# Performance work log

Hardware: AMD Instinct MI355X
Metric: run time of the kernel (lower is better)

## Reference

```python
import jax, jax.numpy as jnp
import numpy as np

B, NQ, NK, D = 8, 2048, 2048, 512

def setup_inputs() -> dict:
    key = jax.random.key(0)
    ks = jax.random.split(key, 6)
    s = 1.0 / np.sqrt(D)
    return {
        "query": jax.random.normal(ks[0], (B, NQ, D), dtype=jnp.float32),
        "key":   jax.random.normal(ks[1], (B, NK, D), dtype=jnp.float32),
        "value": jax.random.normal(ks[2], (B, NK, D), dtype=jnp.float32),
        "Wq": jax.random.normal(ks[3], (D, D), dtype=jnp.float32) * s,
        "Wk": jax.random.normal(ks[4], (D, D), dtype=jnp.float32) * s,
        "Wv": jax.random.normal(ks[5], (D, D), dtype=jnp.float32) * s,
    }

def reference(query, key, value, Wq, Wk, Wv):
    # nn.Linear(bias=False): y = x @ W.T
    q = jnp.einsum('bnd,ed->bne', query, Wq)
    k = jnp.einsum('bnd,ed->bne', key, Wk)
    v = jnp.einsum('bnd,ed->bne', value, Wv)
    # NOTE: original module applies NO 1/sqrt(d) scaling
    scores = jnp.einsum('bqd,bkd->bqk', q, k)   # [B, NQ, NK]
    weights = jax.nn.softmax(scores, axis=-1)
    return jnp.einsum('bqk,bkd->bqd', weights, v)
```

## Files before the change

kernel.cpp:

```cpp
#include <hip/hip_runtime.h>

typedef __attribute__((ext_vector_type(8))) short short8;
typedef __attribute__((ext_vector_type(8))) _Float16 half8;
typedef __attribute__((ext_vector_type(4))) float f32x4;
typedef __attribute__((ext_vector_type(4))) unsigned short u16x4;
typedef __attribute__((ext_vector_type(4))) _Float16 half4;

#define NB 8
#define NQL 2048
#define NKL 2048
#define DD 512

static __device__ __forceinline__ void stage16(const void* g, void* l){
  __builtin_amdgcn_global_load_lds(
      (const __attribute__((address_space(1))) void*)g,
      (__attribute__((address_space(3))) void*)l, 16, 0, 0);
}

static __device__ __forceinline__ void barrier_lgkm(){
  asm volatile("s_waitcnt lgkmcnt(0)" ::: "memory");
  __builtin_amdgcn_s_barrier();
  asm volatile("" ::: "memory");
}

static __device__ __forceinline__ float red4_max(float x){
  float a = x, b = x;
  asm volatile("v_permlane16_swap_b32 %0, %1" : "+v"(a), "+v"(b));
  x = fmaxf(a, b);
  a = x; b = x;
  asm volatile("v_permlane32_swap_b32 %0, %1" : "+v"(a), "+v"(b));
  return fmaxf(a, b);
}
static __device__ __forceinline__ float red4_sum(float x){
  float a = x, b = x;
  asm volatile("v_permlane16_swap_b32 %0, %1" : "+v"(a), "+v"(b));
  x = a + b;
  a = x; b = x;
  asm volatile("v_permlane32_swap_b32 %0, %1" : "+v"(a), "+v"(b));
  return a + b;
}

__global__ __launch_bounds__(256) void split3_k(
    const float* __restrict__ Wq, const float* __restrict__ Wk, const float* __restrict__ Wv,
    _Float16* __restrict__ w16q, _Float16* __restrict__ w16k, _Float16* __restrict__ w16v,
    int n4){
  const int z = blockIdx.y;
  const float* x = (z==0) ? Wq : (z==1) ? Wk : Wv;
  _Float16* o16 = (z==0) ? w16q : (z==1) ? w16k : w16v;
  int i = blockIdx.x*256 + threadIdx.x;
  if (i >= n4) return;
  f32x4 v = reinterpret_cast<const f32x4*>(x)[i];
  half4 h;
  #pragma unroll
  for (int j=0;j<4;j++) h[j] = (_Float16)v[j];
  reinterpret_cast<half4*>(o16)[i] = h;
}

__global__ __launch_bounds__(256, 2) void proj2_k(
    const float* __restrict__ Xq, const float* __restrict__ Xk, const float* __restrict__ Xv,
    const _Float16* __restrict__ W16q, const _Float16* __restrict__ W16k, const _Float16* __restrict__ W16v,
    _Float16* __restrict__ Yqh, _Float16* __restrict__ Yql,
    _Float16* __restrict__ Ykt,
    _Float16* __restrict__ Yvt)
{
  __shared__ _Float16 AB[2][3][128][32];

  const int z = blockIdx.z;
  const float*    X  = (z==0) ? Xq   : (z==1) ? Xk   : Xv;
  const _Float16* Wf = (z==0) ? W16q : (z==1) ? W16k : W16v;

  const int mbase = blockIdx.x * 128;
  const int nbase = blockIdx.y * 128;
  const int tid = threadIdx.x;
  const int w = tid >> 6, lane = tid & 63;
  const int l15 = lane & 15, l4 = lane >> 4;
  const int wr = w >> 1, wc = w & 1;

  const int arow = tid >> 1, ahalf = tid & 1;
  const int brow_l = w*16 + (lane>>2);
  const int bkg    = (lane & 3) ^ ((lane >> 3) & 3);

  f32x4 acc[4][4];
  #pragma unroll
  for (int m=0;m<4;m++)
    #pragma unroll
    for (int n=0;n<4;n++) acc[m][n] = (f32x4){0.f,0.f,0.f,0.f};

  f32x4 xa[4];
  {
    const f32x4* xp = reinterpret_cast<const f32x4*>(X + (size_t)(mbase+arow)*DD + ahalf*16);
    #pragma unroll
    for (int q=0;q<4;q++) xa[q] = xp[q];
  }
  {
    _Float16* lB = &AB[0][2][0][0] + w*512;
    #pragma unroll
    for (int r=0;r<2;r++){
      const size_t gh = (size_t)(nbase + r*64 + brow_l)*DD + bkg*8;
      stage16(Wf + gh, lB + r*2048);
    }
  }
  {
    asm volatile("s_waitcnt vmcnt(2)" ::: "memory");
    half8 h0,h1,l0,l1;
    #pragma unroll
    for (int j=0;j<4;j++){
      float v0 = xa[0][j], v1 = xa[1][j];
      h0[j] = (_Float16)v0; h0[4+j] = (_Float16)v1;
      l0[j] = (_Float16)(v0 - (float)h0[j]); l0[4+j] = (_Float16)(v1 - (float)h0[4+j]);
      float v2 = xa[2][j], v3 = xa[3][j];
      h1[j] = (_Float16)v2; h1[4+j] = (_Float16)v3;
      l1[j] = (_Float16)(v2 - (float)h1[j]); l1[4+j] = (_Float16)(v3 - (float)h1[4+j]);
    }
    const int sw = (arow>>1)&3;
    const int cg0 = (ahalf*2) ^ sw, cg1 = (ahalf*2+1) ^ sw;
    *reinterpret_cast<half8*>(&AB[0][0][arow][cg0*8]) = h0;
    *reinterpret_cast<half8*>(&AB[0][0][arow][cg1*8]) = h1;
    *reinterpret_cast<half8*>(&AB[0][1][arow][cg0*8]) = l0;
    *reinterpret_cast<half8*>(&AB[0][1][arow][cg1*8]) = l1;
  }

  const int asw = (l15>>1)&3;

  #pragma unroll 1
  for (int s=0; s<16; ++s){
    const int cur = s&1, nxt = cur^1;
    asm volatile("s_waitcnt vmcnt(0)" ::: "memory");
    barrier_lgkm();

    if (s < 15){
      const f32x4* xp = reinterpret_cast<const f32x4*>(X + (size_t)(mbase+arow)*DD + (s+1)*32 + ahalf*16);
      #pragma unroll
      for (int q=0;q<4;q++) xa[q] = xp[q];
      _Float16* lB = &AB[nxt][2][0][0] + w*512;
      #pragma unroll
      for (int r=0;r<2;r++){
        const size_t gh = (size_t)(nbase + r*64 + brow_l)*DD + (s+1)*32 + bkg*8;
        stage16(Wf + gh, lB + r*2048);
      }
    }

    half8 ah[4], al[4], wf[4];
    #pragma unroll
    for (int m=0;m<4;m++){
      const int rA = wr*64 + m*16 + l15;
      const int cg = (l4 ^ asw)*8;
      ah[m] = *reinterpret_cast<const half8*>(&AB[cur][0][rA][cg]);
      al[m] = *reinterpret_cast<const half8*>(&AB[cur][1][rA][cg]);
    }
    #pragma unroll
    for (int n=0;n<4;n++){
      const int rB = wc*64 + n*16 + l15;
      const int cg = (l4 ^ asw)*8;
      wf[n] = *reinterpret_cast<const half8*>(&AB[cur][2][rB][cg]);
    }
    #pragma unroll
    for (int m=0;m<4;m++)
      #pragma unroll
      for (int n=0;n<4;n++) acc[m][n] = __builtin_amdgcn_mfma_f32_16x16x32_f16(ah[m], wf[n], acc[m][n], 0,0,0);
    #pragma unroll
    for (int m=0;m<4;m++)
      #pragma unroll
      for (int n=0;n<4;n++) acc[m][n] = __builtin_amdgcn_mfma_f32_16x16x32_f16(al[m], wf[n], acc[m][n], 0,0,0);

    if (s < 15){
      asm volatile("s_waitcnt vmcnt(2)" ::: "memory");
      half8 h0,h1,l0,l1;
      #pragma unroll
      for (int j=0;j<4;j++){
        float v0 = xa[0][j], v1 = xa[1][j];
        h0[j] = (_Float16)v0; h0[4+j] = (_Float16)v1;
        l0[j] = (_Float16)(v0 - (float)h0[j]); l0[4+j] = (_Float16)(v1 - (float)h0[4+j]);
        float v2 = xa[2][j], v3 = xa[3][j];
        h1[j] = (_Float16)v2; h1[4+j] = (_Float16)v3;
        l1[j] = (_Float16)(v2 - (float)h1[j]); l1[4+j] = (_Float16)(v3 - (float)h1[4+j]);
      }
      const int sw = (arow>>1)&3;
      const int cg0 = (ahalf*2) ^ sw, cg1 = (ahalf*2+1) ^ sw;
      *reinterpret_cast<half8*>(&AB[nxt][0][arow][cg0*8]) = h0;
      *reinterpret_cast<half8*>(&AB[nxt][0][arow][cg1*8]) = h1;
      *reinterpret_cast<half8*>(&AB[nxt][1][arow][cg0*8]) = l0;
      *reinterpret_cast<half8*>(&AB[nxt][1][arow][cg1*8]) = l1;
    }
  }

  #pragma unroll
  for (int m=0;m<4;m++){
    #pragma unroll
    for (int n=0;n<4;n++){
      #pragma unroll
      for (int j=0;j<4;j++){
        const int row = mbase + wr*64 + m*16 + l4*4 + j;
        const int col = nbase + wc*64 + n*16 + l15;
        const float y = acc[m][n][j];
        if (z == 0){
          const _Float16 h = (_Float16)y;
          const _Float16 l = (_Float16)(y - (float)h);
          const size_t idx = (size_t)row*DD + col;
          Yqh[idx] = h; Yql[idx] = l;
        } else if (z == 1){
          const int bb = row >> 11, nn = row & 2047, kt = nn >> 5;
          const size_t tb = ((size_t)(bb*64 + kt)) << 14;
          const int kr = nn & 31, cg = col >> 3, ci = col & 7;
          const size_t idx = tb + ((size_t)kr)*512 + (size_t)((((cg ^ (kr & 7)) << 3)) | ci);
          Ykt[idx] = (_Float16)y;
        } else {
          const int bb = row >> 11, nn = row & 2047, kt = nn >> 5;
          const size_t tb = ((size_t)(bb*64 + kt)) << 14;
          const int kk = nn & 31;
          const size_t idx = tb + ((size_t)col)*32 + (size_t)(((((kk >> 3) ^ ((col >> 1) & 3)) << 3)) | (kk & 7));
          Yvt[idx] = (_Float16)y;
        }
      }
    }
  }
}

__global__ __launch_bounds__(512, 2) void attn_k(
    const _Float16* __restrict__ Qh, const _Float16* __restrict__ Ql,
    const _Float16* __restrict__ Kt,
    const _Float16* __restrict__ Vt,
    float* __restrict__ Out)
{
  __shared__ _Float16 K_lds[2][32][512];
  __shared__ _Float16 V_lds[2][512][32];
  __shared__ _Float16 P_s[2][64][40];
  __shared__ float sc_s[2][64];
  __shared__ float l_s[64];

  const int bid = blockIdx.x;
  const int b  = bid & 7;
  const int qt = bid >> 3;
  const int tid = threadIdx.x;
  const int w = tid >> 6, lane = tid & 63;
  const int l15 = lane & 15, l4 = lane >> 4;
  const bool isQK = (w < 4);
  const int qw = w & 3;

  const _Float16* gK = Kt + ((size_t)(b*64) << 14);
  const _Float16* gV = Vt + ((size_t)(b*64) << 14);
  const int goff  = w*512 + lane*8;
  const int lbase = w*512;

  f32x4 r[32];
  float m_old = -1e30f, lacc = 0.f;
  if (isQK){
    const size_t qoff = (size_t)(b*NQL + qt*64 + qw*16 + l15)*DD + l4*8;
    #pragma unroll
    for (int kc=0;kc<16;kc++){
      r[kc]    = __builtin_bit_cast(f32x4, *reinterpret_cast<const half8*>(Qh + qoff + kc*32));
      r[16+kc] = __builtin_bit_cast(f32x4, *reinterpret_cast<const half8*>(Ql + qoff + kc*32));
    }
  } else {
    #pragma unroll
    for (int i=0;i<32;i++) r[i] = (f32x4){0.f,0.f,0.f,0.f};
  }

  {
    _Float16* lK = &K_lds[0][0][0];
    #pragma unroll
    for (int q=0;q<4;q++) stage16(gK + q*4096 + goff, lK + q*4096 + lbase);
  }

  const int kx = l15 & 7;
  const int row_i = qw*16 + l15;

  #pragma unroll 1
  for (int kt=0; kt<64; ++kt){
    const int par = kt & 1;
    asm volatile("s_waitcnt vmcnt(0)" ::: "memory");
    barrier_lgkm();

    if (kt < 63){
      const _Float16* g = gK + ((size_t)(kt+1) << 14);
      _Float16* lK = &K_lds[par^1][0][0];
      #pragma unroll
      for (int q=0;q<4;q++) stage16(g + q*4096 + goff, lK + q*4096 + lbase);
    }
    {
      const _Float16* g = gV + ((size_t)kt << 14);
      _Float16* lV = &V_lds[par][0][0];
      #pragma unroll
      for (int q=0;q<4;q++) stage16(g + q*4096 + goff, lV + q*4096 + lbase);
    }

    if (isQK){
      f32x4 s0h = (f32x4){0.f,0.f,0.f,0.f}, s0l = (f32x4){0.f,0.f,0.f,0.f};
      f32x4 s1h = (f32x4){0.f,0.f,0.f,0.f}, s1l = (f32x4){0.f,0.f,0.f,0.f};
      __builtin_amdgcn_s_setprio(1);
      #pragma unroll
      for (int kc=0;kc<16;kc++){
        const int cg = ((kc*4 + l4) ^ kx) << 3;
        const half8 kf0 = *reinterpret_cast<const half8*>(&K_lds[par][l15][cg]);
        const half8 kf1 = *reinterpret_cast<const half8*>(&K_lds[par][16+l15][cg]);
        const half8 qh = __builtin_bit_cast(half8, r[kc]);
        const half8 ql = __builtin_bit_cast(half8, r[16+kc]);
        s0h = __builtin_amdgcn_mfma_f32_16x16x32_f16(kf0, qh, s0h, 0,0,0);
        s0l = __builtin_amdgcn_mfma_f32_16x16x32_f16(kf0, ql, s0l, 0,0,0);
        s1h = __builtin_amdgcn_mfma_f32_16x16x32_f16(kf1, qh, s1h, 0,0,0);
        s1l = __builtin_amdgcn_mfma_f32_16x16x32_f16(kf1, ql, s1l, 0,0,0);
      }
      __builtin_amdgcn_s_setprio(0);
      const f32x4 sv0 = s0h + s0l;
      const f32x4 sv1 = s1h + s1l;

      float mw = fmaxf(fmaxf(fmaxf(sv0[0],sv0[1]), fmaxf(sv0[2],sv0[3])),
                       fmaxf(fmaxf(sv1[0],sv1[1]), fmaxf(sv1[2],sv1[3])));
      float p0 = __expf(sv0[0]-m_old), p1 = __expf(sv0[1]-m_old);
      float p2 = __expf(sv0[2]-m_old), p3 = __expf(sv0[3]-m_old);
      float p4 = __expf(sv1[0]-m_old), p5 = __expf(sv1[1]-m_old);
      float p6 = __expf(sv1[2]-m_old), p7 = __expf(sv1[3]-m_old);
      mw = red4_max(mw);
      float e_old = 1.0f;
      if (mw > m_old + 8.0f){
        e_old = __expf(m_old - mw);
        p0 = __expf(sv0[0]-mw); p1 = __expf(sv0[1]-mw);
        p2 = __expf(sv0[2]-mw); p3 = __expf(sv0[3]-mw);
        p4 = __expf(sv1[0]-mw); p5 = __expf(sv1[1]-mw);
        p6 = __expf(sv1[2]-mw); p7 = __expf(sv1[3]-mw);
        m_old = mw;
      }
      if (l4 == 0) sc_s[par][row_i] = e_old;
      uint2 hv;
      hv.x = (unsigned)__builtin_bit_cast(unsigned short,(_Float16)p0) |
             ((unsigned)__builtin_bit_cast(unsigned short,(_Float16)p1)<<16);
      hv.y = (unsigned)__builtin_bit_cast(unsigned short,(_Float16)p2) |
             ((unsigned)__builtin_bit_cast(unsigned short,(_Float16)p3)<<16);
      *reinterpret_cast<uint2*>(&P_s[par][row_i][l4*4]) = hv;
      uint2 hw;
      hw.x = (unsigned)__builtin_bit_cast(unsigned short,(_Float16)p4) |
             ((unsigned)__builtin_bit_cast(unsigned short,(_Float16)p5)<<16);
      hw.y = (unsigned)__builtin_bit_cast(unsigned short,(_Float16)p6) |
             ((unsigned)__builtin_bit_cast(unsigned short,(_Float16)p7)<<16);
      *reinterpret_cast<uint2*>(&P_s[par][row_i][16 + l4*4]) = hw;
      float ssum = (p0+p1)+(p2+p3)+((p4+p5)+(p6+p7));
      ssum = red4_sum(ssum);
      lacc = lacc*e_old + ssum;
    } else if (kt > 0){
      const int pp = par^1;
      float scs[4];
      bool need = false;
      #pragma unroll
      for (int j=0;j<4;j++){
        scs[j] = sc_s[pp][qw*16 + l4*4 + j];
        need = need || (scs[j] < 0.999999f);
      }
      if (__any(need)){
        #pragma unroll
        for (int f=0;f<32;f++)
          #pragma unroll
          for (int j=0;j<4;j++) r[f][j] *= scs[j];
      }
      const half8 pa = *reinterpret_cast<const half8*>(&P_s[pp][row_i][l4*8]);
      __builtin_amdgcn_s_setprio(1);
      #pragma unroll
      for (int f=0;f<32;f++){
        const int dcol = f*16 + l15;
        const int vb = (l4 ^ ((dcol>>1)&3)) << 3;
        const half8 vv = *reinterpret_cast<const half8*>(&V_lds[pp][dcol][vb]);
        r[f] = __builtin_amdgcn_mfma_f32_16x16x32_f16(pa, vv, r[f], 0,0,0);
      }
      __builtin_amdgcn_s_setprio(0);
    }
  }

  if (isQK && l4 == 0) l_s[row_i] = lacc;
  asm volatile("s_waitcnt vmcnt(0)" ::: "memory");
  barrier_lgkm();

  if (!isQK){
    float scs[4];
    bool need = false;
    #pragma unroll
    for (int j=0;j<4;j++){
      scs[j] = sc_s[1][qw*16 + l4*4 + j];
      need = need || (scs[j] < 0.999999f);
    }
    if (__any(need)){
      #pragma unroll
      for (int f=0;f<32;f++)
        #pragma unroll
        for (int j=0;j<4;j++) r[f][j] *= scs[j];
    }
    const half8 pa = *reinterpret_cast<const half8*>(&P_s[1][row_i][l4*8]);
    #pragma unroll
    for (int f=0;f<32;f++){
      const int dcol = f*16 + l15;
      const int vb = (l4 ^ ((dcol>>1)&3)) << 3;
      const half8 vv = *reinterpret_cast<const half8*>(&V_lds[1][dcol][vb]);
      r[f] = __builtin_amdgcn_mfma_f32_16x16x32_f16(pa, vv, r[f], 0,0,0);
    }
    float inv[4];
    #pragma unroll
    for (int j=0;j<4;j++) inv[j] = 1.0f / l_s[qw*16 + l4*4 + j];
    #pragma unroll
    for (int j=0;j<4;j++){
      const int row = qw*16 + l4*4 + j;
      const size_t obase = (size_t)(b*NQL + qt*64 + row)*DD;
      #pragma unroll
      for (int f=0;f<32;f++){
        Out[obase + f*16 + l15] = r[f][j]*inv[j];
      }
    }
  }
}

extern "C" void kernel_launch(void* const* d_in, const int* in_sizes, int n_in,
                              void* d_out, int out_size, void* d_ws, size_t ws_size,
                              hipStream_t stream) {
  const float* query = (const float*)d_in[0];
  const float* key   = (const float*)d_in[1];
  const float* value = (const float*)d_in[2];
  const float* Wq    = (const float*)d_in[3];
  const float* Wk    = (const float*)d_in[4];
  const float* Wv    = (const float*)d_in[5];
  float* out = (float*)d_out;

  const size_t SB = (size_t)NB*NQL*DD;
  const size_t WB = (size_t)DD*DD;

  _Float16* p = (_Float16*)d_ws;
  _Float16 *w16q = p, *w16k = p + WB, *w16v = p + 2*WB;
  _Float16* q0 = p + 3*WB;
  _Float16 *qh16 = q0,          *ql16 = q0 + SB;
  _Float16 *Kt16 = q0 + 2*SB;
  _Float16 *Vt16 = q0 + 3*SB;

  dim3 sg(256, 3);
  split3_k<<<sg, 256, 0, stream>>>(Wq, Wk, Wv, w16q, w16k, w16v, (int)(WB/4));

  dim3 pg(128, 4, 3);
  proj2_k<<<pg, 256, 0, stream>>>(query, key, value,
                                  w16q, w16k, w16v,
                                  qh16, ql16, Kt16, Vt16);

  attn_k<<<256, 512, 0, stream>>>(qh16, ql16, Kt16, Vt16, out);
}
```

Baseline: 208.4 us.

## Halve attention query tile, load V directly into registers, drop LDS staging

The attention kernel now uses 32-row query tiles with 256-thread blocks (2 QK waves, 2 PV waves), launching 512 blocks instead of 256. The PV waves each own half of the head dimension and read V fragments straight from global memory into registers, one step ahead, instead of staging them through LDS. The V swizzle in the projection is removed to match. Permlane-swap reductions are replaced with shfl_xor. The aim is to cut LDS traffic and footprint and raise block count, at the cost of each block re-reading K for only half as many query rows and more global V loads per FLOP.

```diff
diff --git a/kernel.cpp b/kernel.cpp
--- a/kernel.cpp
+++ b/kernel.cpp
@@ -21,23 +21,6 @@
   asm volatile("s_waitcnt lgkmcnt(0)" ::: "memory");
   __builtin_amdgcn_s_barrier();
   asm volatile("" ::: "memory");
-}
-
-static __device__ __forceinline__ float red4_max(float x){
-  float a = x, b = x;
-  asm volatile("v_permlane16_swap_b32 %0, %1" : "+v"(a), "+v"(b));
-  x = fmaxf(a, b);
-  a = x; b = x;
-  asm volatile("v_permlane32_swap_b32 %0, %1" : "+v"(a), "+v"(b));
-  return fmaxf(a, b);
-}
-static __device__ __forceinline__ float red4_sum(float x){
-  float a = x, b = x;
-  asm volatile("v_permlane16_swap_b32 %0, %1" : "+v"(a), "+v"(b));
-  x = a + b;
-  a = x; b = x;
-  asm volatile("v_permlane32_swap_b32 %0, %1" : "+v"(a), "+v"(b));
-  return a + b;
 }
 
 __global__ __launch_bounds__(256) void split3_k(
@@ -208,7 +191,7 @@
           const int bb = row >> 11, nn = row & 2047, kt = nn >> 5;
           const size_t tb = ((size_t)(bb*64 + kt)) << 14;
           const int kk = nn & 31;
-          const size_t idx = tb + ((size_t)col)*32 + (size_t)(((((kk >> 3) ^ ((col >> 1) & 3)) << 3)) | (kk & 7));
+          const size_t idx = tb + ((size_t)col)*32 + (size_t)kk;
           Yvt[idx] = (_Float16)y;
         }
       }
@@ -216,17 +199,16 @@
   }
 }
 
-__global__ __launch_bounds__(512, 2) void attn_k(
+__global__ __launch_bounds__(256, 2) void attn_k(
     const _Float16* __restrict__ Qh, const _Float16* __restrict__ Ql,
     const _Float16* __restrict__ Kt,
     const _Float16* __restrict__ Vt,
     float* __restrict__ Out)
 {
   __shared__ _Float16 K_lds[2][32][512];
-  __shared__ _Float16 V_lds[2][512][32];
-  __shared__ _Float16 P_s[2][64][40];
-  __shared__ float sc_s[2][64];
-  __shared__ float l_s[64];
+  __shared__ _Float16 P_s[2][32][40];
+  __shared__ float sc_s[2][32];
+  __shared__ float l_s[32];
 
   const int bid = blockIdx.x;
   const int b  = bid & 7;
@@ -234,8 +216,8 @@
   const int tid = threadIdx.x;
   const int w = tid >> 6, lane = tid & 63;
   const int l15 = lane & 15, l4 = lane >> 4;
-  const bool isQK = (w < 4);
-  const int qw = w & 3;
+  const bool isQK = (w < 2);
+  const int qw = w & 1;
 
   const _Float16* gK = Kt + ((size_t)(b*64) << 14);
   const _Float16* gV = Vt + ((size_t)(b*64) << 14);
@@ -243,9 +225,10 @@
   const int lbase = w*512;
 
   f32x4 r[32];
+  half8 vr[16];
   float m_old = -1e30f, lacc = 0.f;
   if (isQK){
-    const size_t qoff = (size_t)(b*NQL + qt*64 + qw*16 + l15)*DD + l4*8;
+    const size_t qoff = (size_t)(b*NQL + qt*32 + qw*16 + l15)*DD + l4*8;
     #pragma unroll
     for (int kc=0;kc<16;kc++){
       r[kc]    = __builtin_bit_cast(f32x4, *reinterpret_cast<const half8*>(Qh + qoff + kc*32));
@@ -259,11 +242,12 @@
   {
     _Float16* lK = &K_lds[0][0][0];
     #pragma unroll
-    for (int q=0;q<4;q++) stage16(gK + q*4096 + goff, lK + q*4096 + lbase);
+    for (int q=0;q<8;q++) stage16(gK + q*2048 + goff, lK + q*2048 + lbase);
   }
 
   const int kx = l15 & 7;
   const int row_i = qw*16 + l15;
+  const int vcol = qw*256 + l15;
 
   #pragma unroll 1
   for (int kt=0; kt<64; ++kt){
@@ -275,13 +259,7 @@
       const _Float16* g = gK + ((size_t)(kt+1) << 14);
       _Float16* lK = &K_lds[par^1][0][0];
       #pragma unroll
-      for (int q=0;q<4;q++) stage16(g + q*4096 + goff, lK + q*4096 + lbase);
-    }
-    {
-      const _Float16* g = gV + ((size_t)kt << 14);
-      _Float16* lV = &V_lds[par][0][0];
-      #pragma unroll
-      for (int q=0;q<4;q++) stage16(g + q*4096 + goff, lV + q*4096 + lbase);
+      for (int q=0;q<8;q++) stage16(g + q*2048 + goff, lK + q*2048 + lbase);
     }
 
     if (isQK){
@@ -310,7 +288,8 @@
       float p2 = __expf(sv0[2]-m_old), p3 = __expf(sv0[3]-m_old);
       float p4 = __expf(sv1[0]-m_old), p5 = __expf(sv1[1]-m_old);
       float p6 = __expf(sv1[2]-m_old), p7 = __expf(sv1[3]-m_old);
-      mw = red4_max(mw);
+      mw = fmaxf(mw, __shfl_xor(mw, 16));
+      mw = fmaxf(mw, __shfl_xor(mw, 32));
       float e_old = 1.0f;
       if (mw > m_old + 8.0f){
         e_old = __expf(m_old - mw);
@@ -334,33 +313,46 @@
              ((unsigned)__builtin_bit_cast(unsigned short,(_Float16)p7)<<16);
       *reinterpret_cast<uint2*>(&P_s[par][row_i][16 + l4*4]) = hw;
       float ssum = (p0+p1)+(p2+p3)+((p4+p5)+(p6+p7));
-      ssum = red4_sum(ssum);
+      ssum += __shfl_xor(ssum, 16);
+      ssum += __shfl_xor(ssum, 32);
       lacc = lacc*e_old + ssum;
-    } else if (kt > 0){
+    } else {
       const int pp = par^1;
-      float scs[4];
-      bool need = false;
-      #pragma unroll
-      for (int j=0;j<4;j++){
-        scs[j] = sc_s[pp][qw*16 + l4*4 + j];
-        need = need || (scs[j] < 0.999999f);
-      }
-      if (__any(need)){
+      if (kt > 0){
+        float scs[2][4];
+        bool need = false;
         #pragma unroll
-        for (int f=0;f<32;f++)
+        for (int rg=0;rg<2;rg++)
           #pragma unroll
-          for (int j=0;j<4;j++) r[f][j] *= scs[j];
-      }
-      const half8 pa = *reinterpret_cast<const half8*>(&P_s[pp][row_i][l4*8]);
-      __builtin_amdgcn_s_setprio(1);
-      #pragma unroll
-      for (int f=0;f<32;f++){
-        const int dcol = f*16 + l15;
-        const int vb = (l4 ^ ((dcol>>1)&3)) << 3;
-        const half8 vv = *reinterpret_cast<const half8*>(&V_lds[pp][dcol][vb]);
-        r[f] = __builtin_amdgcn_mfma_f32_16x16x32_f16(pa, vv, r[f], 0,0,0);
-      }
-      __builtin_amdgcn_s_setprio(0);
+          for (int j=0;j<4;j++){
+            scs[rg][j] = sc_s[pp][rg*16 + l4*4 + j];
+            need = need || (scs[rg][j] < 0.999999f);
+          }
+        if (__any(need)){
+          #pragma unroll
+          for (int rg=0;rg<2;rg++)
+            #pragma unroll
+            for (int f=0;f<16;f++)
+              #pragma unroll
+              for (int j=0;j<4;j++) r[rg*16+f][j] *= scs[rg][j];
+        }
+        const half8 pa0 = *reinterpret_cast<const half8*>(&P_s[pp][l15][l4*8]);
+        const half8 pa1 = *reinterpret_cast<const half8*>(&P_s[pp][16+l15][l4*8]);
+        __builtin_amdgcn_s_setprio(1);
+        #pragma unroll
+        for (int f=0;f<16;f++){
+          r[f]    = __builtin_amdgcn_mfma_f32_16x16x32_f16(pa0, vr[f], r[f],    0,0,0);
+          r[16+f] = __builtin_amdgcn_mfma_f32_16x16x32_f16(pa1, vr[f], r[16+f], 0,0,0);
+        }
+        __builtin_amdgcn_s_setprio(0);
+      }
+      {
+        const _Float16* g = gV + ((size_t)kt << 14);
+        #pragma unroll
+        for (int f=0;f<16;f++){
+          vr[f] = *reinterpret_cast<const half8*>(g + (size_t)(vcol + f*16)*32 + l4*8);
+        }
+      }
     }
   }
 
@@ -369,37 +361,45 @@
   barrier_lgkm();
 
   if (!isQK){
-    float scs[4];
+    float scs[2][4];
     bool need = false;
     #pragma unroll
-    for (int j=0;j<4;j++){
-      scs[j] = sc_s[1][qw*16 + l4*4 + j];
-      need = need || (scs[j] < 0.999999f);
-    }
+    for (int rg=0;rg<2;rg++)
+      #pragma unroll
+      for (int j=0;j<4;j++){
+        scs[rg][j] = sc_s[1][rg*16 + l4*4 + j];
+        need = need || (scs[rg][j] < 0.999999f);
+      }
     if (__any(need)){
       #pragma unroll
-      for (int f=0;f<32;f++)
+      for (int rg=0;rg<2;rg++)
         #pragma unroll
-        for (int j=0;j<4;j++) r[f][j] *= scs[j];
-    }
-    const half8 pa = *reinterpret_cast<const half8*>(&P_s[1][row_i][l4*8]);
-    #pragma unroll
-    for (int f=0;f<32;f++){
-      const int dcol = f*16 + l15;
-      const int vb = (l4 ^ ((dcol>>1)&3)) << 3;
-      const half8 vv = *reinterpret_cast<const half8*>(&V_lds[1][dcol][vb]);
-      r[f] = __builtin_amdgcn_mfma_f32_16x16x32_f16(pa, vv, r[f], 0,0,0);
-    }
-    float inv[4];
-    #pragma unroll
-    for (int j=0;j<4;j++) inv[j] = 1.0f / l_s[qw*16 + l4*4 + j];
-    #pragma unroll
-    for (int j=0;j<4;j++){
-      const int row = qw*16 + l4*4 + j;
-      const size_t obase = (size_t)(b*NQL + qt*64 + row)*DD;
-      #pragma unroll
-      for (int f=0;f<32;f++){
-        Out[obase + f*16 + l15] = r[f][j]*inv[j];
+        for (int f=0;f<16;f++)
+          #pragma unroll
+          for (int j=0;j<4;j++) r[rg*16+f][j] *= scs[rg][j];
+    }
+    const half8 pa0 = *reinterpret_cast<const half8*>(&P_s[1][l15][l4*8]);
+    const half8 pa1 = *reinterpret_cast<const half8*>(&P_s[1][16+l15][l4*8]);
+    #pragma unroll
+    for (int f=0;f<16;f++){
+      r[f]    = __builtin_amdgcn_mfma_f32_16x16x32_f16(pa0, vr[f], r[f],    0,0,0);
+      r[16+f] = __builtin_amdgcn_mfma_f32_16x16x32_f16(pa1, vr[f], r[16+f], 0,0,0);
+    }
+    float inv[2][4];
+    #pragma unroll
+    for (int rg=0;rg<2;rg++)
+      #pragma unroll
+      for (int j=0;j<4;j++) inv[rg][j] = 1.0f / l_s[rg*16 + l4*4 + j];
+    #pragma unroll
+    for (int rg=0;rg<2;rg++){
+      #pragma unroll
+      for (int j=0;j<4;j++){
+        const int row = rg*16 + l4*4 + j;
+        const size_t obase = (size_t)(b*NQL + qt*32 + row)*DD;
+        #pragma unroll
+        for (int f=0;f<16;f++){
+          Out[obase + qw*256 + f*16 + l15] = r[rg*16+f][j]*inv[rg][j];
+        }
       }
     }
   }
@@ -434,5 +434,5 @@
                                   w16q, w16k, w16v,
                                   qh16, ql16, Kt16, Vt16);
 
-  attn_k<<<256, 512, 0, stream>>>(qh16, ql16, Kt16, Vt16, out);
-}
+  attn_k<<<512, 256, 0, stream>>>(qh16, ql16, Kt16, Vt16, out);
+}
```

After: 225.5 us. +8.2%, slower.
